# Optimization experiments

Measured on AMD Instinct MI355X. Metric: run time of the kernel, lower is better.

## Reference

```python
import jax, jax.numpy as jnp
import numpy as np

B, L, DIM = 2, 1024, 512
HEADS = 8
D = DIM // HEADS
FORE_DIM, POST_DIM = 256, 1024
L_FORE, L_POST = 4 * L, L // 4


def setup_inputs() -> dict:
    key = jax.random.key(0)
    ks = jax.random.split(key, 8)
    s = 0.02  # weight init scale
    return {
        "x": jax.random.normal(ks[0], (B, L, DIM), jnp.float32),
        "fore_x": jax.random.normal(ks[1], (B, L_FORE, FORE_DIM), jnp.float32),
        "post_x": jax.random.normal(ks[2], (B, L_POST, POST_DIM), jnp.float32),
        # Linear weights stored [in, out] (transposed vs torch nn.Linear)
        "wq": jax.random.normal(ks[3], (DIM, DIM), jnp.float32) * s,
        "bq": jnp.zeros((DIM,), jnp.float32),
        "wkv1": jax.random.normal(ks[4], (FORE_DIM, 2 * DIM), jnp.float32) * s,
        "bkv1": jnp.zeros((2 * DIM,), jnp.float32),
        "wkv2": jax.random.normal(ks[5], (POST_DIM, 2 * DIM), jnp.float32) * s,
        "bkv2": jnp.zeros((2 * DIM,), jnp.float32),
        "wproj": jax.random.normal(ks[6], (3 * DIM, DIM), jnp.float32) * s,
        "bproj": jnp.zeros((DIM,), jnp.float32),
    }


def reference(x, fore_x, post_x, wq, bq, wkv1, bkv1, wkv2, bkv2, wproj, bproj):
    scale = D ** (-0.5)
    # q: [B, H, L, D], pre-scaled as in the torch code
    q = (x @ wq + bq).reshape(B, L, HEADS, D).transpose(0, 2, 1, 3) * scale

    def cross_attn(ctx, w, b):
        # ctx: [B, Lc, Cin] -> k, v: [B, H, Lc, D]
        kv = (ctx @ w + b).reshape(B, ctx.shape[1], 2, HEADS, D)
        k = kv[:, :, 0].transpose(0, 2, 1, 3)
        v = kv[:, :, 1].transpose(0, 2, 1, 3)
        attn = jax.nn.softmax(jnp.einsum("bhqd,bhkd->bhqk", q, k), axis=-1)
        out = jnp.einsum("bhqk,bhkd->bhqd", attn, v)
        return out.transpose(0, 2, 1, 3).reshape(B, L, DIM)

    x_2 = cross_attn(post_x, wkv2, bkv2)
    x_1 = cross_attn(fore_x, wkv1, bkv1)
    cat = jnp.concatenate([x, x_1, x_2], axis=2)  # [B, L, 3*DIM]
    return cat @ wproj + bproj
```

## Files before the change

kernel.cpp:

```cpp
#include <hip/hip_runtime.h>
#include <hip/hip_bf16.h>
#include <stdint.h>

typedef __attribute__((ext_vector_type(8))) short bf8;
typedef __attribute__((ext_vector_type(4))) short bf4;
typedef __attribute__((ext_vector_type(2))) short bf2;
typedef __attribute__((ext_vector_type(4))) float f32x4;

__device__ inline short f2bf(float f) {
  union { __hip_bfloat16 h; short s; } u;
  u.h = __float2bfloat16(f);
  return u.s;
}
__device__ inline float bf2f(short s) {
  union { short s; __hip_bfloat16 h; } u;
  u.s = s;
  return __bfloat162float(u.h);
}

__device__ inline f32x4 mfma16(bf8 a, bf8 b, f32x4 c) {
  return __builtin_amdgcn_mfma_f32_16x16x32_bf16(a, b, c, 0, 0, 0);
}

__global__ __launch_bounds__(256) void gemm3_k(
    const float* __restrict__ x, const float* __restrict__ fore,
    const float* __restrict__ post,
    const float* __restrict__ wq, const float* __restrict__ wkv1,
    const float* __restrict__ bkv1, const float* __restrict__ wkv2,
    short* __restrict__ kv1, short* __restrict__ cat,
    short* __restrict__ qpart, short* __restrict__ kv2part)
{
  __shared__ __align__(16) short a_lds[2][128 * 40];
  __shared__ __align__(16) short b_lds[2][64 * 40];

  const int bid = blockIdx.x;
  const float *A, *W, *bias = nullptr;
  short* out;
  int N, lda, ldo, m0, n0, koff;
  bool addb, wcat = false;
  if (bid < 1024) {
    A = fore; W = wkv1; bias = bkv1; out = kv1;
    N = 1024; lda = 256; ldo = 1024; koff = 0;
    m0 = (bid >> 4) * 128; n0 = (bid & 15) * 64; addb = true;
  } else if (bid < 1280) {
    int j = bid - 1024; int kc = j >> 7; j &= 127;
    A = x; W = wq; out = qpart + (size_t)kc * (2048 * 512);
    N = 512; lda = 512; ldo = 512; koff = kc * 256;
    m0 = (j >> 3) * 128; n0 = (j & 7) * 64; addb = false;
    wcat = (j & 7) == 0;
  } else {
    int j = bid - 1280; int kc = j >> 6; j &= 63;
    A = post; W = wkv2; out = kv2part + (size_t)kc * (512 * 1024);
    N = 1024; lda = 1024; ldo = 1024; koff = kc * 256;
    m0 = (j >> 4) * 128; n0 = (j & 15) * 64; addb = false;
  }

  const int tid = threadIdx.x;
  const int w = tid >> 6, lane = tid & 63, g = lane >> 4, lr = lane & 15;
  const int wrow = w & 1, wcol = w >> 1;

  f32x4 z = {0.f, 0.f, 0.f, 0.f};
  f32x4 acc[4][2];
#pragma unroll
  for (int mi = 0; mi < 4; ++mi)
#pragma unroll
    for (int ni = 0; ni < 2; ++ni) acc[mi][ni] = z;

  const int arow = tid >> 3, ac4 = tid & 7;
  const int bcol = tid & 63, bj4 = tid >> 6;

  float4 ra[4], rna[4];
  float rw[8], rnw[8];

  auto LOADA = [&](int kg, float4* af, float* wg) {
#pragma unroll
    for (int i = 0; i < 4; ++i)
      af[i] = *(const float4*)&A[(size_t)(m0 + arow + 32 * i) * lda + kg + ac4 * 4];
#pragma unroll
    for (int j = 0; j < 8; ++j)
      wg[j] = W[(size_t)(kg + bj4 * 8 + j) * N + n0 + bcol];
  };
  auto STAGE = [&](int b, const float4* af, const float* wg, int kg) {
#pragma unroll
    for (int i = 0; i < 4; ++i) {
      int rr = arow + 32 * i;
      int s = (ac4 >> 1) ^ (rr & 3);
      bf4 o;
      o[0] = f2bf(af[i].x); o[1] = f2bf(af[i].y);
      o[2] = f2bf(af[i].z); o[3] = f2bf(af[i].w);
      *(bf4*)&a_lds[b][rr * 40 + s * 8 + (ac4 & 1) * 4] = o;
      if (wcat)
        *(bf4*)&cat[(size_t)(m0 + rr) * 1536 + kg + ac4 * 4] = o;
    }
    int s = bj4 ^ (bcol & 3);
    bf8 o;
#pragma unroll
    for (int j = 0; j < 8; ++j) o[j] = f2bf(wg[j]);
    *(bf8*)&b_lds[b][bcol * 40 + s * 8] = o;
  };

  LOADA(koff, ra, rw);
  STAGE(0, ra, rw, koff);
  LOADA(koff + 32, rna, rnw);
  __syncthreads();

#pragma unroll
  for (int it = 0; it < 8; ++it) {
    if (it < 7) STAGE((it + 1) & 1, rna, rnw, koff + (it + 1) * 32);
    if (it < 6) LOADA(koff + (it + 2) * 32, rna, rnw);

    const int b = it & 1;
    bf8 afr[4], bfr[2];
#pragma unroll
    for (int mi = 0; mi < 4; ++mi) {
      int row = wrow * 64 + mi * 16 + lr;
      afr[mi] = *(const bf8*)&a_lds[b][row * 40 + ((g ^ (row & 3)) << 3)];
    }
#pragma unroll
    for (int ni = 0; ni < 2; ++ni) {
      int col = wcol * 32 + ni * 16 + lr;
      bfr[ni] = *(const bf8*)&b_lds[b][col * 40 + ((g ^ (col & 3)) << 3)];
    }
#pragma unroll
    for (int mi = 0; mi < 4; ++mi)
#pragma unroll
      for (int ni = 0; ni < 2; ++ni)
        acc[mi][ni] = mfma16(afr[mi], bfr[ni], acc[mi][ni]);
    __syncthreads();
  }

#pragma unroll
  for (int ni = 0; ni < 2; ++ni) {
    int col = n0 + wcol * 32 + ni * 16 + lr;
    float bv = addb ? bias[col] : 0.f;
#pragma unroll
    for (int mi = 0; mi < 4; ++mi) {
      int rowb = m0 + wrow * 64 + mi * 16 + g * 4;
#pragma unroll
      for (int r = 0; r < 4; ++r)
        out[(size_t)(rowb + r) * ldo + col] = f2bf(acc[mi][ni][r] + bv);
    }
  }
}

__global__ __launch_bounds__(256) void finalize_k(
    const short* __restrict__ qpart, const short* __restrict__ kv2part,
    const float* __restrict__ bq, const float* __restrict__ bkv2,
    const float* __restrict__ wproj,
    short* __restrict__ qb, short* __restrict__ kv2, short* __restrict__ wT)
{
  __shared__ float tl[64][65];
  const int bid = blockIdx.x, tid = threadIdx.x;
  if (bid < 1024) {
    int i = bid * 256 + tid;
    const float qsc = 0.125f * 1.44269504088896f;
    bf4 a = *(const bf4*)&qpart[(size_t)i * 4];
    bf4 b = *(const bf4*)&qpart[1048576 + (size_t)i * 4];
    int col = (i * 4) & 511;
    bf4 o;
#pragma unroll
    for (int j = 0; j < 4; ++j)
      o[j] = f2bf((bf2f(a[j]) + bf2f(b[j]) + bq[col + j]) * qsc);
    ((bf4*)qb)[i] = o;
  } else if (bid < 1536) {
    int i = (bid - 1024) * 256 + tid;
    bf4 a = *(const bf4*)&kv2part[(size_t)i * 4];
    bf4 b = *(const bf4*)&kv2part[524288 + (size_t)i * 4];
    bf4 c = *(const bf4*)&kv2part[1048576 + (size_t)i * 4];
    bf4 d = *(const bf4*)&kv2part[1572864 + (size_t)i * 4];
    int col = (i * 4) & 1023;
    bf4 o;
#pragma unroll
    for (int j = 0; j < 4; ++j)
      o[j] = f2bf(bf2f(a[j]) + bf2f(b[j]) + bf2f(c[j]) + bf2f(d[j]) + bkv2[col + j]);
    ((bf4*)kv2)[i] = o;
  } else {
    int tb = bid - 1536;
    int kt = tb % 24, nt = tb / 24;
    int k0 = kt * 64, n0 = nt * 64;
    int kr = tid >> 2, c4 = tid & 3;
#pragma unroll
    for (int i = 0; i < 4; ++i) {
      int cc = c4 + i * 4;
      float4 v = *(const float4*)&wproj[(size_t)(k0 + kr) * 512 + n0 + cc * 4];
      tl[kr][cc * 4 + 0] = v.x; tl[kr][cc * 4 + 1] = v.y;
      tl[kr][cc * 4 + 2] = v.z; tl[kr][cc * 4 + 3] = v.w;
    }
    __syncthreads();
    int nr = tid >> 2, p = tid & 3;
#pragma unroll
    for (int i = 0; i < 2; ++i) {
      int kk = p * 16 + i * 8;
      bf8 o;
#pragma unroll
      for (int j = 0; j < 8; ++j) o[j] = f2bf(tl[kk + j][nr]);
      *(bf8*)&wT[(size_t)(n0 + nr) * 1536 + k0 + kk] = o;
    }
  }
}

__global__ __launch_bounds__(256) void gemmo_k(
    const short* __restrict__ A, const short* __restrict__ wT,
    const float* __restrict__ bias, float* __restrict__ out)
{
  __shared__ __align__(16) short a_lds[2][64 * 40];
  __shared__ __align__(16) short b_lds[2][64 * 40];
  const int tid = threadIdx.x;
  const int w = tid >> 6, lane = tid & 63, g = lane >> 4, lr = lane & 15;
  const int id = blockIdx.x;
  const int m = ((id >> 3) & 3) | ((id & 7) << 2);
  const int n = id >> 5;
  const int m0 = m * 64, n0 = n * 64;
  const int K = 1536, N = 512;

  f32x4 z = {0.f, 0.f, 0.f, 0.f};
  f32x4 acc[4];
#pragma unroll
  for (int mi = 0; mi < 4; ++mi) acc[mi] = z;

  const int arow = tid >> 2, ac8 = tid & 3;
  const int bcol = tid & 63, bj4 = tid >> 6;
  bf8 ra, rna, rb, rnb;

  auto LOADAB = [&](int kg, bf8& ab, bf8& bb) {
    ab = *(const bf8*)&A[(size_t)(m0 + arow) * K + kg + ac8 * 8];
    bb = *(const bf8*)&wT[(size_t)(n0 + bcol) * K + kg + bj4 * 8];
  };
  auto STAGE = [&](int b, bf8 ab, bf8 bb) {
    *(bf8*)&a_lds[b][arow * 40 + ((ac8 ^ (arow & 3)) << 3)] = ab;
    *(bf8*)&b_lds[b][bcol * 40 + ((bj4 ^ (bcol & 3)) << 3)] = bb;
  };

  const int nit = K >> 5;
  LOADAB(0, ra, rb);
  STAGE(0, ra, rb);
  LOADAB(32, rna, rnb);
  __syncthreads();

  for (int it = 0; it < nit; ++it) {
    if (it + 1 < nit) STAGE((it + 1) & 1, rna, rnb);
    if (it + 2 < nit) LOADAB((it + 2) * 32, rna, rnb);

    const int b = it & 1;
    bf8 afr[4], bfr;
#pragma unroll
    for (int mi = 0; mi < 4; ++mi) {
      int row = mi * 16 + lr;
      afr[mi] = *(const bf8*)&a_lds[b][row * 40 + ((g ^ (row & 3)) << 3)];
    }
    {
      int col = w * 16 + lr;
      bfr = *(const bf8*)&b_lds[b][col * 40 + ((g ^ (col & 3)) << 3)];
    }
#pragma unroll
    for (int mi = 0; mi < 4; ++mi) acc[mi] = mfma16(afr[mi], bfr, acc[mi]);
    __syncthreads();
  }

  {
    int col = n0 + w * 16 + lr;
    float bv = bias[col];
#pragma unroll
    for (int mi = 0; mi < 4; ++mi) {
      int rowb = m0 + mi * 16 + g * 4;
#pragma unroll
      for (int r = 0; r < 4; ++r)
        out[(size_t)(rowb + r) * 512 + col] = acc[mi][r] + bv;
    }
  }
}

__global__ __launch_bounds__(256) void attn_k(
    const short* __restrict__ q,
    const short* __restrict__ kv1, const short* __restrict__ kv2,
    short* __restrict__ o1, float* __restrict__ l1,
    short* __restrict__ o2, float* __restrict__ l2)
{
  __shared__ __align__(16) short k_lds[64 * 64];
  __shared__ __align__(16) short v_lds[64 * 72];
  const int tid = threadIdx.x;
  const int w = tid >> 6, lane = tid & 63, g = lane >> 4, lr = lane & 15;

  const int bid = blockIdx.x;
  const short* kvsrc;
  short* opart;
  float* lpart;
  int qt, h, bb, split, chunk, Lc;
  if (bid < 1024) {
    qt = bid >> 7; int j = bid & 127;
    h = j & 7; int zz = j >> 3;
    bb = zz >> 3; split = zz & 7;
    kvsrc = kv1; opart = o1; lpart = l1; chunk = 512; Lc = 4096;
  } else {
    int j2 = bid - 1024;
    qt = j2 >> 6; int r = j2 & 63;
    h = r & 7; int zz = r >> 3;
    bb = zz >> 2; split = zz & 3;
    kvsrc = kv2; opart = o2; lpart = l2; chunk = 64; Lc = 256;
  }

  const int qbase = bb * 1024 + qt * 128 + w * 32;
  bf8 qfA[2], qfB[2];
#pragma unroll
  for (int s2 = 0; s2 < 2; ++s2) {
    const short* qp = &q[(size_t)(qbase + s2 * 16 + lr) * 512 + h * 64];
    qfA[s2] = *(const bf8*)&qp[g * 8];
    qfB[s2] = *(const bf8*)&qp[32 + g * 8];
  }

  const f32x4 z = {0.f, 0.f, 0.f, 0.f};
  f32x4 oaccT[2][4];
#pragma unroll
  for (int s2 = 0; s2 < 2; ++s2)
#pragma unroll
    for (int i = 0; i < 4; ++i) oaccT[s2][i] = z;
  float lsum_l[2] = {0.f, 0.f};

  const short* kvb = kvsrc + (size_t)bb * Lc * 1024 + (size_t)split * chunk * 1024;

  const int krow = tid >> 2, ksl = tid & 3;
  const short* kgp = kvb + (size_t)krow * 1024 + h * 64;
  const int vi = tid & 31, vj = tid >> 5;
  const short* vgp = kvb + (size_t)(2 * vi) * 1024 + 512 + h * 64 + vj * 8;
  const int lc0 = 2 * vi;
  const int vpos = (lc0 & 32) + ((lc0 & 12) << 1) + ((lc0 & 16) >> 2) + (lc0 & 3);

  bf8 k0c, k1c, v0c, v1c;
  k0c = *(const bf8*)(kgp + ksl * 8);
  k1c = *(const bf8*)(kgp + (ksl + 4) * 8);
  v0c = *(const bf8*)vgp;
  v1c = *(const bf8*)(vgp + 1024);

  const int nit = chunk >> 6;
  for (int it = 0; it < nit; ++it) {
    __syncthreads();
    *(bf8*)&k_lds[krow * 64 + ((ksl ^ (krow & 7)) << 3)] = k0c;
    *(bf8*)&k_lds[krow * 64 + (((ksl + 4) ^ (krow & 7)) << 3)] = k1c;
#pragma unroll
    for (int jj = 0; jj < 8; ++jj) {
      int d = vj * 8 + jj;
      bf2 pr; pr[0] = v0c[jj]; pr[1] = v1c[jj];
      *(bf2*)&v_lds[d * 72 + vpos] = pr;
    }
    __syncthreads();
    if (it + 1 < nit) {
      size_t off = (size_t)64 * 1024 * (it + 1);
      k0c = *(const bf8*)(kgp + off + ksl * 8);
      k1c = *(const bf8*)(kgp + off + (ksl + 4) * 8);
      v0c = *(const bf8*)(vgp + off);
      v1c = *(const bf8*)(vgp + off + 1024);
    }

    f32x4 sv[2][4];
#pragma unroll
    for (int t = 0; t < 4; ++t) {
      int lc = t * 16 + lr;
      bf8 kf0 = *(const bf8*)&k_lds[lc * 64 + ((g ^ (lc & 7)) << 3)];
      bf8 kf1 = *(const bf8*)&k_lds[lc * 64 + (((4 + g) ^ (lc & 7)) << 3)];
#pragma unroll
      for (int s2 = 0; s2 < 2; ++s2) {
        sv[s2][t] = mfma16(kf0, qfA[s2], z);
        sv[s2][t] = mfma16(kf1, qfB[s2], sv[s2][t]);
      }
    }

    bf8 pb[2][2];
#pragma unroll
    for (int s2 = 0; s2 < 2; ++s2) {
      float acc_l = 0.f;
#pragma unroll
      for (int t = 0; t < 4; ++t) {
        float p0 = exp2f(sv[s2][t][0]);
        float p1 = exp2f(sv[s2][t][1]);
        float p2 = exp2f(sv[s2][t][2]);
        float p3 = exp2f(sv[s2][t][3]);
        acc_l += (p0 + p1) + (p2 + p3);
        int c = t >> 1, hb = (t & 1) * 4;
        pb[s2][c][hb + 0] = f2bf(p0);
        pb[s2][c][hb + 1] = f2bf(p1);
        pb[s2][c][hb + 2] = f2bf(p2);
        pb[s2][c][hb + 3] = f2bf(p3);
      }
      lsum_l[s2] += acc_l;
    }

#pragma unroll
    for (int dt = 0; dt < 4; ++dt) {
      int d = dt * 16 + lr;
      bf8 vf0 = *(const bf8*)&v_lds[d * 72 + 8 * g];
      bf8 vf1 = *(const bf8*)&v_lds[d * 72 + 32 + 8 * g];
      oaccT[0][dt] = mfma16(vf0, pb[0][0], oaccT[0][dt]);
      oaccT[0][dt] = mfma16(vf1, pb[0][1], oaccT[0][dt]);
      oaccT[1][dt] = mfma16(vf0, pb[1][0], oaccT[1][dt]);
      oaccT[1][dt] = mfma16(vf1, pb[1][1], oaccT[1][dt]);
    }
  }

#pragma unroll
  for (int s2 = 0; s2 < 2; ++s2) {
    int prow = (bb * 8 + h) * 1024 + qt * 128 + w * 32 + s2 * 16 + lr;
    short* ob = opart + ((size_t)split * 16384 + prow) * 64;
#pragma unroll
    for (int dt = 0; dt < 4; ++dt) {
      bf4 o4;
#pragma unroll
      for (int r = 0; r < 4; ++r) o4[r] = f2bf(oaccT[s2][dt][r]);
      *(bf4*)&ob[dt * 16 + 4 * g] = o4;
    }
    float t = lsum_l[s2];
    t += __shfl_xor(t, 16);
    t += __shfl_xor(t, 32);
    if (g == 0) lpart[(size_t)split * 16384 + prow] = t;
  }
}

__global__ __launch_bounds__(256) void comb_k(
    const short* __restrict__ o1, const float* __restrict__ l1,
    const short* __restrict__ o2, const float* __restrict__ l2,
    short* __restrict__ cat)
{
  int row = blockIdx.x * 4 + (threadIdx.x >> 6);
  int d = threadIdx.x & 63;
  int bb = row >> 13, h = (row >> 10) & 7, qr = row & 1023;
  short* crow = &cat[(size_t)(bb * 1024 + qr) * 1536 + h * 64 + d];

  float o = 0.f, l = 0.f;
#pragma unroll
  for (int s = 0; s < 8; ++s) {
    o += bf2f(o1[((size_t)s * 16384 + row) * 64 + d]);
    l += l1[(size_t)s * 16384 + row];
  }
  crow[512] = f2bf(o / l);

  o = 0.f; l = 0.f;
#pragma unroll
  for (int s = 0; s < 4; ++s) {
    o += bf2f(o2[((size_t)s * 16384 + row) * 64 + d]);
    l += l2[(size_t)s * 16384 + row];
  }
  crow[1024] = f2bf(o / l);
}

extern "C" void kernel_launch(void* const* d_in, const int* in_sizes, int n_in,
                              void* d_out, int out_size, void* d_ws, size_t ws_size,
                              hipStream_t stream) {
  const float* x     = (const float*)d_in[0];
  const float* fore  = (const float*)d_in[1];
  const float* post  = (const float*)d_in[2];
  const float* wq    = (const float*)d_in[3];
  const float* bq    = (const float*)d_in[4];
  const float* wkv1  = (const float*)d_in[5];
  const float* bkv1  = (const float*)d_in[6];
  const float* wkv2  = (const float*)d_in[7];
  const float* bkv2  = (const float*)d_in[8];
  const float* wproj = (const float*)d_in[9];
  const float* bproj = (const float*)d_in[10];

  char* ws = (char*)d_ws;
  short* qb      = (short*)ws;
  short* kv1     = (short*)(ws + (2ull << 20));
  short* kv2     = (short*)(ws + (18ull << 20));
  short* cat     = (short*)(ws + (19ull << 20));
  short* o1      = (short*)(ws + (25ull << 20));
  short* o2      = (short*)(ws + (41ull << 20));
  float* l1      = (float*)(ws + (49ull << 20));
  float* l2      = (float*)(ws + (49ull << 20) + 524288);
  short* qpart   = (short*)(ws + (50ull << 20));
  short* kv2part = (short*)(ws + (52ull << 20));
  short* wT      = (short*)(ws + (56ull << 20));

  gemm3_k<<<1536, 256, 0, stream>>>(x, fore, post, wq, wkv1, bkv1, wkv2,
                                    kv1, cat, qpart, kv2part);
  finalize_k<<<1728, 256, 0, stream>>>(qpart, kv2part, bq, bkv2, wproj,
                                       qb, kv2, wT);
  attn_k<<<1536, 256, 0, stream>>>(qb, kv1, kv2, o1, l1, o2, l2);
  comb_k<<<4096, 256, 0, stream>>>(o1, l1, o2, l2, cat);
  gemmo_k<<<256, 256, 0, stream>>>(cat, wT, bproj, (float*)d_out);
}
```

Before: 91.20 us.

## Fuse split-K reductions into producer kernels via last-block atomic counters

Removes the separate finalize and combine kernels. The wproj transpose moves into the first GEMM launch as extra blocks. Each split-K tile now writes fp32 partials and bumps an atomic counter, and the last-arriving block reduces the partials, adds bias and scale, and writes bf16 q/kv2. The attention kernel does the same for its split-softmax partials and writes straight into the concat buffer. This drops two launches and their global round-trips, at the cost of a memset, fp32 partial traffic and serialized tail work in the last blocks.

```diff
diff --git a/kernel.cpp b/kernel.cpp
--- a/kernel.cpp
+++ b/kernel.cpp
@@ -22,40 +22,72 @@
   return __builtin_amdgcn_mfma_f32_16x16x32_bf16(a, b, c, 0, 0, 0);
 }
 
-__global__ __launch_bounds__(256) void gemm3_k(
+__global__ __launch_bounds__(256) void mega1_k(
     const float* __restrict__ x, const float* __restrict__ fore,
     const float* __restrict__ post,
-    const float* __restrict__ wq, const float* __restrict__ wkv1,
-    const float* __restrict__ bkv1, const float* __restrict__ wkv2,
+    const float* __restrict__ wq, const float* __restrict__ bq,
+    const float* __restrict__ wkv1, const float* __restrict__ bkv1,
+    const float* __restrict__ wkv2, const float* __restrict__ bkv2,
+    const float* __restrict__ wproj,
     short* __restrict__ kv1, short* __restrict__ cat,
-    short* __restrict__ qpart, short* __restrict__ kv2part)
+    float* __restrict__ qpart, float* __restrict__ kv2part,
+    short* __restrict__ qb, short* __restrict__ kv2, short* __restrict__ wT,
+    int* __restrict__ cnt)
 {
   __shared__ __align__(16) short a_lds[2][128 * 40];
   __shared__ __align__(16) short b_lds[2][64 * 40];
-
-  const int bid = blockIdx.x;
+  __shared__ int s_old;
+  const int bid = blockIdx.x, tid = threadIdx.x;
+
+  if (bid >= 1536) {
+    float (*tl)[65] = reinterpret_cast<float(*)[65]>(&a_lds[0][0]);
+    int tb = bid - 1536;
+    int kt = tb % 24, nt = tb / 24;
+    int k0 = kt * 64, n0 = nt * 64;
+    int kr = tid >> 2, c4 = tid & 3;
+#pragma unroll
+    for (int i = 0; i < 4; ++i) {
+      int cc = c4 + i * 4;
+      float4 v = *(const float4*)&wproj[(size_t)(k0 + kr) * 512 + n0 + cc * 4];
+      tl[kr][cc * 4 + 0] = v.x; tl[kr][cc * 4 + 1] = v.y;
+      tl[kr][cc * 4 + 2] = v.z; tl[kr][cc * 4 + 3] = v.w;
+    }
+    __syncthreads();
+    int nr = tid >> 2, p = tid & 3;
+#pragma unroll
+    for (int i = 0; i < 2; ++i) {
+      int kk = p * 16 + i * 8;
+      bf8 o;
+#pragma unroll
+      for (int j = 0; j < 8; ++j) o[j] = f2bf(tl[kk + j][nr]);
+      *(bf8*)&wT[(size_t)(n0 + nr) * 1536 + k0 + kk] = o;
+    }
+    return;
+  }
+
   const float *A, *W, *bias = nullptr;
-  short* out;
-  int N, lda, ldo, m0, n0, koff;
-  bool addb, wcat = false;
+  short* out = nullptr;
+  float* outf = nullptr;
+  int N, lda, ldo, m0, n0, koff, tile = -1, nchunk = 0;
+  bool wcat = false;
   if (bid < 1024) {
     A = fore; W = wkv1; bias = bkv1; out = kv1;
     N = 1024; lda = 256; ldo = 1024; koff = 0;
-    m0 = (bid >> 4) * 128; n0 = (bid & 15) * 64; addb = true;
+    m0 = (bid >> 4) * 128; n0 = (bid & 15) * 64;
   } else if (bid < 1280) {
     int j = bid - 1024; int kc = j >> 7; j &= 127;
-    A = x; W = wq; out = qpart + (size_t)kc * (2048 * 512);
+    A = x; W = wq; outf = qpart + (size_t)kc * (2048 * 512);
     N = 512; lda = 512; ldo = 512; koff = kc * 256;
-    m0 = (j >> 3) * 128; n0 = (j & 7) * 64; addb = false;
-    wcat = (j & 7) == 0;
+    m0 = (j >> 3) * 128; n0 = (j & 7) * 64;
+    wcat = (j & 7) == 0; tile = j; nchunk = 2;
   } else {
     int j = bid - 1280; int kc = j >> 6; j &= 63;
-    A = post; W = wkv2; out = kv2part + (size_t)kc * (512 * 1024);
+    A = post; W = wkv2; outf = kv2part + (size_t)kc * (512 * 1024);
     N = 1024; lda = 1024; ldo = 1024; koff = kc * 256;
-    m0 = (j >> 4) * 128; n0 = (j & 15) * 64; addb = false;
-  }
-
-  const int tid = threadIdx.x;
+    m0 = (j >> 4) * 128; n0 = (j & 15) * 64;
+    tile = 128 + j; nchunk = 4;
+  }
+
   const int w = tid >> 6, lane = tid & 63, g = lane >> 4, lr = lane & 15;
   const int wrow = w & 1, wcol = w >> 1;
 
@@ -132,140 +164,60 @@
 #pragma unroll
   for (int ni = 0; ni < 2; ++ni) {
     int col = n0 + wcol * 32 + ni * 16 + lr;
-    float bv = addb ? bias[col] : 0.f;
+    float bv = (tile < 0) ? bias[col] : 0.f;
 #pragma unroll
     for (int mi = 0; mi < 4; ++mi) {
       int rowb = m0 + wrow * 64 + mi * 16 + g * 4;
 #pragma unroll
-      for (int r = 0; r < 4; ++r)
-        out[(size_t)(rowb + r) * ldo + col] = f2bf(acc[mi][ni][r] + bv);
-    }
-  }
-}
-
-__global__ __launch_bounds__(256) void finalize_k(
-    const short* __restrict__ qpart, const short* __restrict__ kv2part,
-    const float* __restrict__ bq, const float* __restrict__ bkv2,
-    const float* __restrict__ wproj,
-    short* __restrict__ qb, short* __restrict__ kv2, short* __restrict__ wT)
-{
-  __shared__ float tl[64][65];
-  const int bid = blockIdx.x, tid = threadIdx.x;
-  if (bid < 1024) {
-    int i = bid * 256 + tid;
+      for (int r = 0; r < 4; ++r) {
+        float val = acc[mi][ni][r] + bv;
+        if (tile < 0)
+          out[(size_t)(rowb + r) * ldo + col] = f2bf(val);
+        else
+          outf[(size_t)(rowb + r) * ldo + col] = val;
+      }
+    }
+  }
+
+  if (tile < 0) return;
+
+  __syncthreads();
+  if (tid == 0) { __threadfence(); s_old = atomicAdd(&cnt[tile], 1); }
+  __syncthreads();
+  if (s_old != nchunk - 1) return;
+  __threadfence();
+
+  const int c4 = (tid & 15) * 4, r0 = tid >> 4;
+  if (nchunk == 2) {
     const float qsc = 0.125f * 1.44269504088896f;
-    bf4 a = *(const bf4*)&qpart[(size_t)i * 4];
-    bf4 b = *(const bf4*)&qpart[1048576 + (size_t)i * 4];
-    int col = (i * 4) & 511;
-    bf4 o;
-#pragma unroll
-    for (int j = 0; j < 4; ++j)
-      o[j] = f2bf((bf2f(a[j]) + bf2f(b[j]) + bq[col + j]) * qsc);
-    ((bf4*)qb)[i] = o;
-  } else if (bid < 1536) {
-    int i = (bid - 1024) * 256 + tid;
-    bf4 a = *(const bf4*)&kv2part[(size_t)i * 4];
-    bf4 b = *(const bf4*)&kv2part[524288 + (size_t)i * 4];
-    bf4 c = *(const bf4*)&kv2part[1048576 + (size_t)i * 4];
-    bf4 d = *(const bf4*)&kv2part[1572864 + (size_t)i * 4];
-    int col = (i * 4) & 1023;
-    bf4 o;
-#pragma unroll
-    for (int j = 0; j < 4; ++j)
-      o[j] = f2bf(bf2f(a[j]) + bf2f(b[j]) + bf2f(c[j]) + bf2f(d[j]) + bkv2[col + j]);
-    ((bf4*)kv2)[i] = o;
+#pragma unroll
+    for (int pass = 0; pass < 8; ++pass) {
+      int row = m0 + r0 + pass * 16;
+      float4 a = *(const float4*)&qpart[(size_t)row * 512 + n0 + c4];
+      float4 b = *(const float4*)&qpart[1048576 + (size_t)row * 512 + n0 + c4];
+      float4 bv = *(const float4*)&bq[n0 + c4];
+      bf4 o;
+      o[0] = f2bf((a.x + b.x + bv.x) * qsc);
+      o[1] = f2bf((a.y + b.y + bv.y) * qsc);
+      o[2] = f2bf((a.z + b.z + bv.z) * qsc);
+      o[3] = f2bf((a.w + b.w + bv.w) * qsc);
+      *(bf4*)&qb[(size_t)row * 512 + n0 + c4] = o;
+    }
   } else {
-    int tb = bid - 1536;
-    int kt = tb % 24, nt = tb / 24;
-    int k0 = kt * 64, n0 = nt * 64;
-    int kr = tid >> 2, c4 = tid & 3;
-#pragma unroll
-    for (int i = 0; i < 4; ++i) {
-      int cc = c4 + i * 4;
-      float4 v = *(const float4*)&wproj[(size_t)(k0 + kr) * 512 + n0 + cc * 4];
-      tl[kr][cc * 4 + 0] = v.x; tl[kr][cc * 4 + 1] = v.y;
-      tl[kr][cc * 4 + 2] = v.z; tl[kr][cc * 4 + 3] = v.w;
-    }
-    __syncthreads();
-    int nr = tid >> 2, p = tid & 3;
-#pragma unroll
-    for (int i = 0; i < 2; ++i) {
-      int kk = p * 16 + i * 8;
-      bf8 o;
-#pragma unroll
-      for (int j = 0; j < 8; ++j) o[j] = f2bf(tl[kk + j][nr]);
-      *(bf8*)&wT[(size_t)(n0 + nr) * 1536 + k0 + kk] = o;
-    }
-  }
-}
-
-__global__ __launch_bounds__(256) void gemmo_k(
-    const short* __restrict__ A, const short* __restrict__ wT,
-    const float* __restrict__ bias, float* __restrict__ out)
-{
-  __shared__ __align__(16) short a_lds[2][64 * 40];
-  __shared__ __align__(16) short b_lds[2][64 * 40];
-  const int tid = threadIdx.x;
-  const int w = tid >> 6, lane = tid & 63, g = lane >> 4, lr = lane & 15;
-  const int id = blockIdx.x;
-  const int m = ((id >> 3) & 3) | ((id & 7) << 2);
-  const int n = id >> 5;
-  const int m0 = m * 64, n0 = n * 64;
-  const int K = 1536, N = 512;
-
-  f32x4 z = {0.f, 0.f, 0.f, 0.f};
-  f32x4 acc[4];
-#pragma unroll
-  for (int mi = 0; mi < 4; ++mi) acc[mi] = z;
-
-  const int arow = tid >> 2, ac8 = tid & 3;
-  const int bcol = tid & 63, bj4 = tid >> 6;
-  bf8 ra, rna, rb, rnb;
-
-  auto LOADAB = [&](int kg, bf8& ab, bf8& bb) {
-    ab = *(const bf8*)&A[(size_t)(m0 + arow) * K + kg + ac8 * 8];
-    bb = *(const bf8*)&wT[(size_t)(n0 + bcol) * K + kg + bj4 * 8];
-  };
-  auto STAGE = [&](int b, bf8 ab, bf8 bb) {
-    *(bf8*)&a_lds[b][arow * 40 + ((ac8 ^ (arow & 3)) << 3)] = ab;
-    *(bf8*)&b_lds[b][bcol * 40 + ((bj4 ^ (bcol & 3)) << 3)] = bb;
-  };
-
-  const int nit = K >> 5;
-  LOADAB(0, ra, rb);
-  STAGE(0, ra, rb);
-  LOADAB(32, rna, rnb);
-  __syncthreads();
-
-  for (int it = 0; it < nit; ++it) {
-    if (it + 1 < nit) STAGE((it + 1) & 1, rna, rnb);
-    if (it + 2 < nit) LOADAB((it + 2) * 32, rna, rnb);
-
-    const int b = it & 1;
-    bf8 afr[4], bfr;
-#pragma unroll
-    for (int mi = 0; mi < 4; ++mi) {
-      int row = mi * 16 + lr;
-      afr[mi] = *(const bf8*)&a_lds[b][row * 40 + ((g ^ (row & 3)) << 3)];
-    }
-    {
-      int col = w * 16 + lr;
-      bfr = *(const bf8*)&b_lds[b][col * 40 + ((g ^ (col & 3)) << 3)];
-    }
-#pragma unroll
-    for (int mi = 0; mi < 4; ++mi) acc[mi] = mfma16(afr[mi], bfr, acc[mi]);
-    __syncthreads();
-  }
-
-  {
-    int col = n0 + w * 16 + lr;
-    float bv = bias[col];
-#pragma unroll
-    for (int mi = 0; mi < 4; ++mi) {
-      int rowb = m0 + mi * 16 + g * 4;
-#pragma unroll
-      for (int r = 0; r < 4; ++r)
-        out[(size_t)(rowb + r) * 512 + col] = acc[mi][r] + bv;
+#pragma unroll
+    for (int pass = 0; pass < 8; ++pass) {
+      int row = m0 + r0 + pass * 16;
+      float4 a = *(const float4*)&kv2part[(size_t)row * 1024 + n0 + c4];
+      float4 b = *(const float4*)&kv2part[524288 + (size_t)row * 1024 + n0 + c4];
+      float4 c = *(const float4*)&kv2part[1048576 + (size_t)row * 1024 + n0 + c4];
+      float4 d = *(const float4*)&kv2part[1572864 + (size_t)row * 1024 + n0 + c4];
+      float4 bv = *(const float4*)&bkv2[n0 + c4];
+      bf4 o;
+      o[0] = f2bf(a.x + b.x + c.x + d.x + bv.x);
+      o[1] = f2bf(a.y + b.y + c.y + d.y + bv.y);
+      o[2] = f2bf(a.z + b.z + c.z + d.z + bv.z);
+      o[3] = f2bf(a.w + b.w + c.w + d.w + bv.w);
+      *(bf4*)&kv2[(size_t)row * 1024 + n0 + c4] = o;
     }
   }
 }
@@ -274,10 +226,12 @@
     const short* __restrict__ q,
     const short* __restrict__ kv1, const short* __restrict__ kv2,
     short* __restrict__ o1, float* __restrict__ l1,
-    short* __restrict__ o2, float* __restrict__ l2)
+    short* __restrict__ o2, float* __restrict__ l2,
+    short* __restrict__ cat, int* __restrict__ cnt)
 {
   __shared__ __align__(16) short k_lds[64 * 64];
   __shared__ __align__(16) short v_lds[64 * 72];
+  __shared__ int s_old;
   const int tid = threadIdx.x;
   const int w = tid >> 6, lane = tid & 63, g = lane >> 4, lr = lane & 15;
 
@@ -285,18 +239,22 @@
   const short* kvsrc;
   short* opart;
   float* lpart;
-  int qt, h, bb, split, chunk, Lc;
+  int qt, h, bb, split, chunk, Lc, nsplit, ocol, gidc;
   if (bid < 1024) {
     qt = bid >> 7; int j = bid & 127;
     h = j & 7; int zz = j >> 3;
     bb = zz >> 3; split = zz & 7;
     kvsrc = kv1; opart = o1; lpart = l1; chunk = 512; Lc = 4096;
+    nsplit = 8; ocol = 512;
+    gidc = 192 + (bb * 8 + h) * 8 + qt;
   } else {
     int j2 = bid - 1024;
     qt = j2 >> 6; int r = j2 & 63;
     h = r & 7; int zz = r >> 3;
     bb = zz >> 2; split = zz & 3;
     kvsrc = kv2; opart = o2; lpart = l2; chunk = 64; Lc = 256;
+    nsplit = 4; ocol = 1024;
+    gidc = 320 + (bb * 8 + h) * 8 + qt;
   }
 
   const int qbase = bb * 1024 + qt * 128 + w * 32;
@@ -412,33 +370,103 @@
     t += __shfl_xor(t, 32);
     if (g == 0) lpart[(size_t)split * 16384 + prow] = t;
   }
-}
-
-__global__ __launch_bounds__(256) void comb_k(
-    const short* __restrict__ o1, const float* __restrict__ l1,
-    const short* __restrict__ o2, const float* __restrict__ l2,
-    short* __restrict__ cat)
+
+  __syncthreads();
+  if (tid == 0) { __threadfence(); s_old = atomicAdd(&cnt[gidc], 1); }
+  __syncthreads();
+  if (s_old != nsplit - 1) return;
+  __threadfence();
+
+  const int prow_grp = (bb * 8 + h) * 1024 + qt * 128;
+  const int d4 = (tid & 15) * 4, rl0 = tid >> 4;
+#pragma unroll
+  for (int pass = 0; pass < 8; ++pass) {
+    int rl = rl0 + pass * 16;
+    int prow = prow_grp + rl;
+    float l = 0.f;
+    for (int s = 0; s < nsplit; ++s) l += lpart[(size_t)s * 16384 + prow];
+    float o0 = 0.f, o1v = 0.f, o2v = 0.f, o3v = 0.f;
+    for (int s = 0; s < nsplit; ++s) {
+      bf4 v = *(const bf4*)&opart[((size_t)s * 16384 + prow) * 64 + d4];
+      o0 += bf2f(v[0]); o1v += bf2f(v[1]); o2v += bf2f(v[2]); o3v += bf2f(v[3]);
+    }
+    float rle = 1.f / l;
+    bf4 o;
+    o[0] = f2bf(o0 * rle); o[1] = f2bf(o1v * rle);
+    o[2] = f2bf(o2v * rle); o[3] = f2bf(o3v * rle);
+    *(bf4*)&cat[(size_t)(bb * 1024 + qt * 128 + rl) * 1536 + ocol + h * 64 + d4] = o;
+  }
+}
+
+__global__ __launch_bounds__(256) void gemmo_k(
+    const short* __restrict__ A, const short* __restrict__ wT,
+    const float* __restrict__ bias, float* __restrict__ out)
 {
-  int row = blockIdx.x * 4 + (threadIdx.x >> 6);
-  int d = threadIdx.x & 63;
-  int bb = row >> 13, h = (row >> 10) & 7, qr = row & 1023;
-  short* crow = &cat[(size_t)(bb * 1024 + qr) * 1536 + h * 64 + d];
-
-  float o = 0.f, l = 0.f;
-#pragma unroll
-  for (int s = 0; s < 8; ++s) {
-    o += bf2f(o1[((size_t)s * 16384 + row) * 64 + d]);
-    l += l1[(size_t)s * 16384 + row];
-  }
-  crow[512] = f2bf(o / l);
-
-  o = 0.f; l = 0.f;
-#pragma unroll
-  for (int s = 0; s < 4; ++s) {
-    o += bf2f(o2[((size_t)s * 16384 + row) * 64 + d]);
-    l += l2[(size_t)s * 16384 + row];
-  }
-  crow[1024] = f2bf(o / l);
+  __shared__ __align__(16) short a_lds[2][64 * 40];
+  __shared__ __align__(16) short b_lds[2][64 * 40];
+  const int tid = threadIdx.x;
+  const int w = tid >> 6, lane = tid & 63, g = lane >> 4, lr = lane & 15;
+  const int id = blockIdx.x;
+  const int m = ((id >> 3) & 3) | ((id & 7) << 2);
+  const int n = id >> 5;
+  const int m0 = m * 64, n0 = n * 64;
+  const int K = 1536;
+
+  f32x4 z = {0.f, 0.f, 0.f, 0.f};
+  f32x4 acc[4];
+#pragma unroll
+  for (int mi = 0; mi < 4; ++mi) acc[mi] = z;
+
+  const int arow = tid >> 2, ac8 = tid & 3;
+  const int bcol = tid & 63, bj4 = tid >> 6;
+  bf8 ra, rna, rb, rnb;
+
+  auto LOADAB = [&](int kg, bf8& ab, bf8& bb) {
+    ab = *(const bf8*)&A[(size_t)(m0 + arow) * K + kg + ac8 * 8];
+    bb = *(const bf8*)&wT[(size_t)(n0 + bcol) * K + kg + bj4 * 8];
+  };
+  auto STAGE = [&](int b, bf8 ab, bf8 bb) {
+    *(bf8*)&a_lds[b][arow * 40 + ((ac8 ^ (arow & 3)) << 3)] = ab;
+    *(bf8*)&b_lds[b][bcol * 40 + ((bj4 ^ (bcol & 3)) << 3)] = bb;
+  };
+
+  const int nit = K >> 5;
+  LOADAB(0, ra, rb);
+  STAGE(0, ra, rb);
+  LOADAB(32, rna, rnb);
+  __syncthreads();
+
+  for (int it = 0; it < nit; ++it) {
+    if (it + 1 < nit) STAGE((it + 1) & 1, rna, rnb);
+    if (it + 2 < nit) LOADAB((it + 2) * 32, rna, rnb);
+
+    const int b = it & 1;
+    bf8 afr[4], bfr;
+#pragma unroll
+    for (int mi = 0; mi < 4; ++mi) {
+      int row = mi * 16 + lr;
+      afr[mi] = *(const bf8*)&a_lds[b][row * 40 + ((g ^ (row & 3)) << 3)];
+    }
+    {
+      int col = w * 16 + lr;
+      bfr = *(const bf8*)&b_lds[b][col * 40 + ((g ^ (col & 3)) << 3)];
+    }
+#pragma unroll
+    for (int mi = 0; mi < 4; ++mi) acc[mi] = mfma16(afr[mi], bfr, acc[mi]);
+    __syncthreads();
+  }
+
+  {
+    int col = n0 + w * 16 + lr;
+    float bv = bias[col];
+#pragma unroll
+    for (int mi = 0; mi < 4; ++mi) {
+      int rowb = m0 + mi * 16 + g * 4;
+#pragma unroll
+      for (int r = 0; r < 4; ++r)
+        out[(size_t)(rowb + r) * 512 + col] = acc[mi][r] + bv;
+    }
+  }
 }
 
 extern "C" void kernel_launch(void* const* d_in, const int* in_sizes, int n_in,
@@ -465,15 +493,15 @@
   short* o2      = (short*)(ws + (41ull << 20));
   float* l1      = (float*)(ws + (49ull << 20));
   float* l2      = (float*)(ws + (49ull << 20) + 524288);
-  short* qpart   = (short*)(ws + (50ull << 20));
-  short* kv2part = (short*)(ws + (52ull << 20));
-  short* wT      = (short*)(ws + (56ull << 20));
-
-  gemm3_k<<<1536, 256, 0, stream>>>(x, fore, post, wq, wkv1, bkv1, wkv2,
-                                    kv1, cat, qpart, kv2part);
-  finalize_k<<<1728, 256, 0, stream>>>(qpart, kv2part, bq, bkv2, wproj,
-                                       qb, kv2, wT);
-  attn_k<<<1536, 256, 0, stream>>>(qb, kv1, kv2, o1, l1, o2, l2);
-  comb_k<<<4096, 256, 0, stream>>>(o1, l1, o2, l2, cat);
+  float* qpart   = (float*)(ws + (50ull << 20));
+  float* kv2part = (float*)(ws + (58ull << 20));
+  short* wT      = (short*)(ws + (66ull << 20));
+  int*   cnt     = (int*)(ws + (68ull << 20));
+
+  hipMemsetAsync(cnt, 0, 448 * sizeof(int), stream);
+  mega1_k<<<1728, 256, 0, stream>>>(x, fore, post, wq, bq, wkv1, bkv1,
+                                    wkv2, bkv2, wproj, kv1, cat,
+                                    qpart, kv2part, qb, kv2, wT, cnt);
+  attn_k<<<1536, 256, 0, stream>>>(qb, kv1, kv2, o1, l1, o2, l2, cat, cnt);
   gemmo_k<<<256, 256, 0, stream>>>(cat, wT, bproj, (float*)d_out);
 }
```

New measurement: 252.6 us. +176.9%, slower.

## Restructure pipeline: fold wproj transpose into GEMM, cut attention splits, direct post-attn write

Applied to the files above, without the earlier changes.

Moves the wproj transpose/convert into the first GEMM launch as extra blocks, and switches the split-K partials for q and kv2 from bf16 to fp32. The post-context attention now runs unsplit and writes normalized output straight into the concat buffer, dropping its partial buffers and combine step. The fore-context attention goes from 8 to 4 splits, with a vectorized combine kernel. This cuts partial-buffer traffic and combine work, but leaves fewer attention blocks (640 vs 1536), which may hurt occupancy, and the fp32 partials double the bytes written and read for those buffers.

```diff
diff --git a/kernel.cpp b/kernel.cpp
--- a/kernel.cpp
+++ b/kernel.cpp
@@ -22,40 +22,68 @@
   return __builtin_amdgcn_mfma_f32_16x16x32_bf16(a, b, c, 0, 0, 0);
 }
 
-__global__ __launch_bounds__(256) void gemm3_k(
+__global__ __launch_bounds__(256) void mega1_k(
     const float* __restrict__ x, const float* __restrict__ fore,
     const float* __restrict__ post,
     const float* __restrict__ wq, const float* __restrict__ wkv1,
     const float* __restrict__ bkv1, const float* __restrict__ wkv2,
+    const float* __restrict__ wproj,
     short* __restrict__ kv1, short* __restrict__ cat,
-    short* __restrict__ qpart, short* __restrict__ kv2part)
+    float* __restrict__ qpart, float* __restrict__ kv2part,
+    short* __restrict__ wT)
 {
   __shared__ __align__(16) short a_lds[2][128 * 40];
   __shared__ __align__(16) short b_lds[2][64 * 40];
-
-  const int bid = blockIdx.x;
+  const int bid = blockIdx.x, tid = threadIdx.x;
+
+  if (bid >= 1536) {
+    float (*tl)[65] = reinterpret_cast<float(*)[65]>(&a_lds[0][0]);
+    int tb = bid - 1536;
+    int kt = tb % 24, nt = tb / 24;
+    int k0 = kt * 64, n0 = nt * 64;
+    int kr = tid >> 2, c4 = tid & 3;
+#pragma unroll
+    for (int i = 0; i < 4; ++i) {
+      int cc = c4 + i * 4;
+      float4 v = *(const float4*)&wproj[(size_t)(k0 + kr) * 512 + n0 + cc * 4];
+      tl[kr][cc * 4 + 0] = v.x; tl[kr][cc * 4 + 1] = v.y;
+      tl[kr][cc * 4 + 2] = v.z; tl[kr][cc * 4 + 3] = v.w;
+    }
+    __syncthreads();
+    int nr = tid >> 2, p = tid & 3;
+#pragma unroll
+    for (int i = 0; i < 2; ++i) {
+      int kk = p * 16 + i * 8;
+      bf8 o;
+#pragma unroll
+      for (int j = 0; j < 8; ++j) o[j] = f2bf(tl[kk + j][nr]);
+      *(bf8*)&wT[(size_t)(n0 + nr) * 1536 + k0 + kk] = o;
+    }
+    return;
+  }
+
   const float *A, *W, *bias = nullptr;
-  short* out;
+  short* out = nullptr;
+  float* outf = nullptr;
   int N, lda, ldo, m0, n0, koff;
-  bool addb, wcat = false;
+  bool wcat = false, bf16out;
   if (bid < 1024) {
     A = fore; W = wkv1; bias = bkv1; out = kv1;
     N = 1024; lda = 256; ldo = 1024; koff = 0;
-    m0 = (bid >> 4) * 128; n0 = (bid & 15) * 64; addb = true;
+    m0 = (bid >> 4) * 128; n0 = (bid & 15) * 64; bf16out = true;
   } else if (bid < 1280) {
     int j = bid - 1024; int kc = j >> 7; j &= 127;
-    A = x; W = wq; out = qpart + (size_t)kc * (2048 * 512);
+    A = x; W = wq; outf = qpart + (size_t)kc * (2048 * 512);
     N = 512; lda = 512; ldo = 512; koff = kc * 256;
-    m0 = (j >> 3) * 128; n0 = (j & 7) * 64; addb = false;
+    m0 = (j >> 3) * 128; n0 = (j & 7) * 64; bf16out = false;
     wcat = (j & 7) == 0;
   } else {
     int j = bid - 1280; int kc = j >> 6; j &= 63;
-    A = post; W = wkv2; out = kv2part + (size_t)kc * (512 * 1024);
+    A = post; W = wkv2; outf = kv2part + (size_t)kc * (512 * 1024);
     N = 1024; lda = 1024; ldo = 1024; koff = kc * 256;
-    m0 = (j >> 4) * 128; n0 = (j & 15) * 64; addb = false;
-  }
-
-  const int tid = threadIdx.x;
+    m0 = (j >> 4) * 128; n0 = (j & 15) * 64; bf16out = false;
+  }
+
   const int w = tid >> 6, lane = tid & 63, g = lane >> 4, lr = lane & 15;
   const int wrow = w & 1, wcol = w >> 1;
 
@@ -132,141 +160,55 @@
 #pragma unroll
   for (int ni = 0; ni < 2; ++ni) {
     int col = n0 + wcol * 32 + ni * 16 + lr;
-    float bv = addb ? bias[col] : 0.f;
+    float bv = bf16out ? bias[col] : 0.f;
 #pragma unroll
     for (int mi = 0; mi < 4; ++mi) {
       int rowb = m0 + wrow * 64 + mi * 16 + g * 4;
 #pragma unroll
-      for (int r = 0; r < 4; ++r)
-        out[(size_t)(rowb + r) * ldo + col] = f2bf(acc[mi][ni][r] + bv);
+      for (int r = 0; r < 4; ++r) {
+        float val = acc[mi][ni][r] + bv;
+        if (bf16out)
+          out[(size_t)(rowb + r) * ldo + col] = f2bf(val);
+        else
+          outf[(size_t)(rowb + r) * ldo + col] = val;
+      }
     }
   }
 }
 
 __global__ __launch_bounds__(256) void finalize_k(
-    const short* __restrict__ qpart, const short* __restrict__ kv2part,
+    const float* __restrict__ qpart, const float* __restrict__ kv2part,
     const float* __restrict__ bq, const float* __restrict__ bkv2,
-    const float* __restrict__ wproj,
-    short* __restrict__ qb, short* __restrict__ kv2, short* __restrict__ wT)
+    short* __restrict__ qb, short* __restrict__ kv2)
 {
-  __shared__ float tl[64][65];
   const int bid = blockIdx.x, tid = threadIdx.x;
   if (bid < 1024) {
     int i = bid * 256 + tid;
     const float qsc = 0.125f * 1.44269504088896f;
-    bf4 a = *(const bf4*)&qpart[(size_t)i * 4];
-    bf4 b = *(const bf4*)&qpart[1048576 + (size_t)i * 4];
+    float4 a = ((const float4*)qpart)[i];
+    float4 b = ((const float4*)qpart)[i + 262144];
     int col = (i * 4) & 511;
+    float4 bv = *(const float4*)&bq[col];
     bf4 o;
-#pragma unroll
-    for (int j = 0; j < 4; ++j)
-      o[j] = f2bf((bf2f(a[j]) + bf2f(b[j]) + bq[col + j]) * qsc);
+    o[0] = f2bf((a.x + b.x + bv.x) * qsc);
+    o[1] = f2bf((a.y + b.y + bv.y) * qsc);
+    o[2] = f2bf((a.z + b.z + bv.z) * qsc);
+    o[3] = f2bf((a.w + b.w + bv.w) * qsc);
     ((bf4*)qb)[i] = o;
-  } else if (bid < 1536) {
-    int i = (bid - 1024) * 256 + tid;
-    bf4 a = *(const bf4*)&kv2part[(size_t)i * 4];
-    bf4 b = *(const bf4*)&kv2part[524288 + (size_t)i * 4];
-    bf4 c = *(const bf4*)&kv2part[1048576 + (size_t)i * 4];
-    bf4 d = *(const bf4*)&kv2part[1572864 + (size_t)i * 4];
-    int col = (i * 4) & 1023;
+  } else {
+    int j = (bid - 1024) * 256 + tid;
+    float4 a = ((const float4*)kv2part)[j];
+    float4 b = ((const float4*)kv2part)[j + 131072];
+    float4 c = ((const float4*)kv2part)[j + 262144];
+    float4 d = ((const float4*)kv2part)[j + 393216];
+    int col = (j * 4) & 1023;
+    float4 bv = *(const float4*)&bkv2[col];
     bf4 o;
-#pragma unroll
-    for (int j = 0; j < 4; ++j)
-      o[j] = f2bf(bf2f(a[j]) + bf2f(b[j]) + bf2f(c[j]) + bf2f(d[j]) + bkv2[col + j]);
-    ((bf4*)kv2)[i] = o;
-  } else {
-    int tb = bid - 1536;
-    int kt = tb % 24, nt = tb / 24;
-    int k0 = kt * 64, n0 = nt * 64;
-    int kr = tid >> 2, c4 = tid & 3;
-#pragma unroll
-    for (int i = 0; i < 4; ++i) {
-      int cc = c4 + i * 4;
-      float4 v = *(const float4*)&wproj[(size_t)(k0 + kr) * 512 + n0 + cc * 4];
-      tl[kr][cc * 4 + 0] = v.x; tl[kr][cc * 4 + 1] = v.y;
-      tl[kr][cc * 4 + 2] = v.z; tl[kr][cc * 4 + 3] = v.w;
-    }
-    __syncthreads();
-    int nr = tid >> 2, p = tid & 3;
-#pragma unroll
-    for (int i = 0; i < 2; ++i) {
-      int kk = p * 16 + i * 8;
-      bf8 o;
-#pragma unroll
-      for (int j = 0; j < 8; ++j) o[j] = f2bf(tl[kk + j][nr]);
-      *(bf8*)&wT[(size_t)(n0 + nr) * 1536 + k0 + kk] = o;
-    }
-  }
-}
-
-__global__ __launch_bounds__(256) void gemmo_k(
-    const short* __restrict__ A, const short* __restrict__ wT,
-    const float* __restrict__ bias, float* __restrict__ out)
-{
-  __shared__ __align__(16) short a_lds[2][64 * 40];
-  __shared__ __align__(16) short b_lds[2][64 * 40];
-  const int tid = threadIdx.x;
-  const int w = tid >> 6, lane = tid & 63, g = lane >> 4, lr = lane & 15;
-  const int id = blockIdx.x;
-  const int m = ((id >> 3) & 3) | ((id & 7) << 2);
-  const int n = id >> 5;
-  const int m0 = m * 64, n0 = n * 64;
-  const int K = 1536, N = 512;
-
-  f32x4 z = {0.f, 0.f, 0.f, 0.f};
-  f32x4 acc[4];
-#pragma unroll
-  for (int mi = 0; mi < 4; ++mi) acc[mi] = z;
-
-  const int arow = tid >> 2, ac8 = tid & 3;
-  const int bcol = tid & 63, bj4 = tid >> 6;
-  bf8 ra, rna, rb, rnb;
-
-  auto LOADAB = [&](int kg, bf8& ab, bf8& bb) {
-    ab = *(const bf8*)&A[(size_t)(m0 + arow) * K + kg + ac8 * 8];
-    bb = *(const bf8*)&wT[(size_t)(n0 + bcol) * K + kg + bj4 * 8];
-  };
-  auto STAGE = [&](int b, bf8 ab, bf8 bb) {
-    *(bf8*)&a_lds[b][arow * 40 + ((ac8 ^ (arow & 3)) << 3)] = ab;
-    *(bf8*)&b_lds[b][bcol * 40 + ((bj4 ^ (bcol & 3)) << 3)] = bb;
-  };
-
-  const int nit = K >> 5;
-  LOADAB(0, ra, rb);
-  STAGE(0, ra, rb);
-  LOADAB(32, rna, rnb);
-  __syncthreads();
-
-  for (int it = 0; it < nit; ++it) {
-    if (it + 1 < nit) STAGE((it + 1) & 1, rna, rnb);
-    if (it + 2 < nit) LOADAB((it + 2) * 32, rna, rnb);
-
-    const int b = it & 1;
-    bf8 afr[4], bfr;
-#pragma unroll
-    for (int mi = 0; mi < 4; ++mi) {
-      int row = mi * 16 + lr;
-      afr[mi] = *(const bf8*)&a_lds[b][row * 40 + ((g ^ (row & 3)) << 3)];
-    }
-    {
-      int col = w * 16 + lr;
-      bfr = *(const bf8*)&b_lds[b][col * 40 + ((g ^ (col & 3)) << 3)];
-    }
-#pragma unroll
-    for (int mi = 0; mi < 4; ++mi) acc[mi] = mfma16(afr[mi], bfr, acc[mi]);
-    __syncthreads();
-  }
-
-  {
-    int col = n0 + w * 16 + lr;
-    float bv = bias[col];
-#pragma unroll
-    for (int mi = 0; mi < 4; ++mi) {
-      int rowb = m0 + mi * 16 + g * 4;
-#pragma unroll
-      for (int r = 0; r < 4; ++r)
-        out[(size_t)(rowb + r) * 512 + col] = acc[mi][r] + bv;
-    }
+    o[0] = f2bf(a.x + b.x + c.x + d.x + bv.x);
+    o[1] = f2bf(a.y + b.y + c.y + d.y + bv.y);
+    o[2] = f2bf(a.z + b.z + c.z + d.z + bv.z);
+    o[3] = f2bf(a.w + b.w + c.w + d.w + bv.w);
+    ((bf4*)kv2)[j] = o;
   }
 }
 
@@ -274,7 +216,7 @@
     const short* __restrict__ q,
     const short* __restrict__ kv1, const short* __restrict__ kv2,
     short* __restrict__ o1, float* __restrict__ l1,
-    short* __restrict__ o2, float* __restrict__ l2)
+    short* __restrict__ cat)
 {
   __shared__ __align__(16) short k_lds[64 * 64];
   __shared__ __align__(16) short v_lds[64 * 72];
@@ -283,20 +225,18 @@
 
   const int bid = blockIdx.x;
   const short* kvsrc;
-  short* opart;
-  float* lpart;
   int qt, h, bb, split, chunk, Lc;
-  if (bid < 1024) {
-    qt = bid >> 7; int j = bid & 127;
+  bool direct;
+  if (bid < 512) {
+    qt = bid >> 6; int j = bid & 63;
     h = j & 7; int zz = j >> 3;
-    bb = zz >> 3; split = zz & 7;
-    kvsrc = kv1; opart = o1; lpart = l1; chunk = 512; Lc = 4096;
+    bb = zz >> 2; split = zz & 3;
+    kvsrc = kv1; chunk = 1024; Lc = 4096; direct = false;
   } else {
-    int j2 = bid - 1024;
-    qt = j2 >> 6; int r = j2 & 63;
-    h = r & 7; int zz = r >> 3;
-    bb = zz >> 2; split = zz & 3;
-    kvsrc = kv2; opart = o2; lpart = l2; chunk = 64; Lc = 256;
+    int j2 = bid - 512;
+    qt = j2 >> 4; int r = j2 & 15;
+    h = r & 7; bb = r >> 3; split = 0;
+    kvsrc = kv2; chunk = 256; Lc = 256; direct = true;
   }
 
   const int qbase = bb * 1024 + qt * 128 + w * 32;
@@ -396,10 +336,29 @@
     }
   }
 
+  if (direct) {
+#pragma unroll
+    for (int s2 = 0; s2 < 2; ++s2) {
+      float t = lsum_l[s2];
+      t += __shfl_xor(t, 16);
+      t += __shfl_xor(t, 32);
+      float rle = 1.f / t;
+      int qrow = qbase + s2 * 16 + lr;
+#pragma unroll
+      for (int dt = 0; dt < 4; ++dt) {
+        bf4 o4;
+#pragma unroll
+        for (int r = 0; r < 4; ++r) o4[r] = f2bf(oaccT[s2][dt][r] * rle);
+        *(bf4*)&cat[(size_t)qrow * 1536 + 1024 + h * 64 + dt * 16 + 4 * g] = o4;
+      }
+    }
+    return;
+  }
+
 #pragma unroll
   for (int s2 = 0; s2 < 2; ++s2) {
     int prow = (bb * 8 + h) * 1024 + qt * 128 + w * 32 + s2 * 16 + lr;
-    short* ob = opart + ((size_t)split * 16384 + prow) * 64;
+    short* ob = o1 + ((size_t)split * 16384 + prow) * 64;
 #pragma unroll
     for (int dt = 0; dt < 4; ++dt) {
       bf4 o4;
@@ -410,35 +369,103 @@
     float t = lsum_l[s2];
     t += __shfl_xor(t, 16);
     t += __shfl_xor(t, 32);
-    if (g == 0) lpart[(size_t)split * 16384 + prow] = t;
+    if (g == 0) l1[(size_t)split * 16384 + prow] = t;
   }
 }
 
 __global__ __launch_bounds__(256) void comb_k(
     const short* __restrict__ o1, const float* __restrict__ l1,
-    const short* __restrict__ o2, const float* __restrict__ l2,
     short* __restrict__ cat)
 {
-  int row = blockIdx.x * 4 + (threadIdx.x >> 6);
-  int d = threadIdx.x & 63;
+  int row = blockIdx.x * 32 + (threadIdx.x >> 3);
+  int d8 = (threadIdx.x & 7) * 8;
+  float l = 0.f;
+#pragma unroll
+  for (int s = 0; s < 4; ++s) l += l1[(size_t)s * 16384 + row];
+  float acc[8] = {};
+#pragma unroll
+  for (int s = 0; s < 4; ++s) {
+    bf8 v = *(const bf8*)&o1[((size_t)s * 16384 + row) * 64 + d8];
+#pragma unroll
+    for (int j = 0; j < 8; ++j) acc[j] += bf2f(v[j]);
+  }
+  float rle = 1.f / l;
+  bf8 o;
+#pragma unroll
+  for (int j = 0; j < 8; ++j) o[j] = f2bf(acc[j] * rle);
   int bb = row >> 13, h = (row >> 10) & 7, qr = row & 1023;
-  short* crow = &cat[(size_t)(bb * 1024 + qr) * 1536 + h * 64 + d];
-
-  float o = 0.f, l = 0.f;
-#pragma unroll
-  for (int s = 0; s < 8; ++s) {
-    o += bf2f(o1[((size_t)s * 16384 + row) * 64 + d]);
-    l += l1[(size_t)s * 16384 + row];
-  }
-  crow[512] = f2bf(o / l);
-
-  o = 0.f; l = 0.f;
-#pragma unroll
-  for (int s = 0; s < 4; ++s) {
-    o += bf2f(o2[((size_t)s * 16384 + row) * 64 + d]);
-    l += l2[(size_t)s * 16384 + row];
-  }
-  crow[1024] = f2bf(o / l);
+  *(bf8*)&cat[(size_t)(bb * 1024 + qr) * 1536 + 512 + h * 64 + d8] = o;
+}
+
+__global__ __launch_bounds__(256) void gemmo_k(
+    const short* __restrict__ A, const short* __restrict__ wT,
+    const float* __restrict__ bias, float* __restrict__ out)
+{
+  __shared__ __align__(16) short a_lds[2][64 * 40];
+  __shared__ __align__(16) short b_lds[2][64 * 40];
+  const int tid = threadIdx.x;
+  const int w = tid >> 6, lane = tid & 63, g = lane >> 4, lr = lane & 15;
+  const int id = blockIdx.x;
+  const int m = ((id >> 3) & 3) | ((id & 7) << 2);
+  const int n = id >> 5;
+  const int m0 = m * 64, n0 = n * 64;
+  const int K = 1536;
+
+  f32x4 z = {0.f, 0.f, 0.f, 0.f};
+  f32x4 acc[4];
+#pragma unroll
+  for (int mi = 0; mi < 4; ++mi) acc[mi] = z;
+
+  const int arow = tid >> 2, ac8 = tid & 3;
+  const int bcol = tid & 63, bj4 = tid >> 6;
+  bf8 ra, rna, rb, rnb;
+
+  auto LOADAB = [&](int kg, bf8& ab, bf8& bb) {
+    ab = *(const bf8*)&A[(size_t)(m0 + arow) * K + kg + ac8 * 8];
+    bb = *(const bf8*)&wT[(size_t)(n0 + bcol) * K + kg + bj4 * 8];
+  };
+  auto STAGE = [&](int b, bf8 ab, bf8 bb) {
+    *(bf8*)&a_lds[b][arow * 40 + ((ac8 ^ (arow & 3)) << 3)] = ab;
+    *(bf8*)&b_lds[b][bcol * 40 + ((bj4 ^ (bcol & 3)) << 3)] = bb;
+  };
+
+  const int nit = K >> 5;
+  LOADAB(0, ra, rb);
+  STAGE(0, ra, rb);
+  LOADAB(32, rna, rnb);
+  __syncthreads();
+
+  for (int it = 0; it < nit; ++it) {
+    if (it + 1 < nit) STAGE((it + 1) & 1, rna, rnb);
+    if (it + 2 < nit) LOADAB((it + 2) * 32, rna, rnb);
+
+    const int b = it & 1;
+    bf8 afr[4], bfr;
+#pragma unroll
+    for (int mi = 0; mi < 4; ++mi) {
+      int row = mi * 16 + lr;
+      afr[mi] = *(const bf8*)&a_lds[b][row * 40 + ((g ^ (row & 3)) << 3)];
+    }
+    {
+      int col = w * 16 + lr;
+      bfr = *(const bf8*)&b_lds[b][col * 40 + ((g ^ (col & 3)) << 3)];
+    }
+#pragma unroll
+    for (int mi = 0; mi < 4; ++mi) acc[mi] = mfma16(afr[mi], bfr, acc[mi]);
+    __syncthreads();
+  }
+
+  {
+    int col = n0 + w * 16 + lr;
+    float bv = bias[col];
+#pragma unroll
+    for (int mi = 0; mi < 4; ++mi) {
+      int rowb = m0 + mi * 16 + g * 4;
+#pragma unroll
+      for (int r = 0; r < 4; ++r)
+        out[(size_t)(rowb + r) * 512 + col] = acc[mi][r] + bv;
+    }
+  }
 }
 
 extern "C" void kernel_launch(void* const* d_in, const int* in_sizes, int n_in,
@@ -462,18 +489,15 @@
   short* kv2     = (short*)(ws + (18ull << 20));
   short* cat     = (short*)(ws + (19ull << 20));
   short* o1      = (short*)(ws + (25ull << 20));
-  short* o2      = (short*)(ws + (41ull << 20));
-  float* l1      = (float*)(ws + (49ull << 20));
-  float* l2      = (float*)(ws + (49ull << 20) + 524288);
-  short* qpart   = (short*)(ws + (50ull << 20));
-  short* kv2part = (short*)(ws + (52ull << 20));
-  short* wT      = (short*)(ws + (56ull << 20));
-
-  gemm3_k<<<1536, 256, 0, stream>>>(x, fore, post, wq, wkv1, bkv1, wkv2,
-                                    kv1, cat, qpart, kv2part);
-  finalize_k<<<1728, 256, 0, stream>>>(qpart, kv2part, bq, bkv2, wproj,
-                                       qb, kv2, wT);
-  attn_k<<<1536, 256, 0, stream>>>(qb, kv1, kv2, o1, l1, o2, l2);
-  comb_k<<<4096, 256, 0, stream>>>(o1, l1, o2, l2, cat);
+  float* l1      = (float*)(ws + (33ull << 20));
+  float* qpart   = (float*)(ws + (34ull << 20));
+  float* kv2part = (float*)(ws + (42ull << 20));
+  short* wT      = (short*)(ws + (50ull << 20));
+
+  mega1_k<<<1728, 256, 0, stream>>>(x, fore, post, wq, wkv1, bkv1, wkv2,
+                                    wproj, kv1, cat, qpart, kv2part, wT);
+  finalize_k<<<1536, 256, 0, stream>>>(qpart, kv2part, bq, bkv2, qb, kv2);
+  attn_k<<<640, 256, 0, stream>>>(qb, kv1, kv2, o1, l1, cat);
+  comb_k<<<512, 256, 0, stream>>>(o1, l1, cat);
   gemmo_k<<<256, 256, 0, stream>>>(cat, wT, bproj, (float*)d_out);
 }
```

Result: slower. 93.17 us (+2.2%).
